# Kernel tuning notes

Measured on AMD Instinct MI355X. Metric: run time of the kernel, lower is better.

Reference implementation:

```python
import jax, jax.numpy as jnp
import numpy as np

# Fixed query graph: 3 terms, 3 predicates, edges (head_term, tail_term, pred):
# (0,1,0), (1,2,1), (0,2,2) -> every term has degree 2 -> seq_len 3 incl. self.
T, P, B, D, H, NL, FF = 3, 3, 16384, 256, 8, 2, 1024
DH = D // H
SCALE = DH ** -0.5


def setup_inputs() -> dict:
    key = jax.random.key(0)
    ks = jax.random.split(key, 8)
    s = 0.02
    f = jnp.float32
    return {
        "term_embs": jax.random.normal(ks[0], (T, B, D), f),
        "pred_embs": jax.random.normal(ks[1], (P, B, D), f),
        "Wq": jax.random.normal(ks[2], (NL, D, D), f) * s,
        "Wk": jax.random.normal(ks[3], (NL, D, D), f) * s,
        "Wv": jax.random.normal(ks[4], (NL, D, D), f) * s,
        "Wo": jax.random.normal(ks[5], (NL, D, D), f) * s,
        "bq": jnp.zeros((NL, D), f),
        "bk": jnp.zeros((NL, D), f),
        "bv": jnp.zeros((NL, D), f),
        "bo": jnp.zeros((NL, D), f),
        "ln1_g": jnp.ones((NL, D), f),
        "ln1_b": jnp.zeros((NL, D), f),
        "ln2_g": jnp.ones((NL, D), f),
        "ln2_b": jnp.zeros((NL, D), f),
        "W1": jax.random.normal(ks[6], (NL, D, FF), f) * s,
        "b1": jnp.zeros((NL, FF), f),
        "W2": jax.random.normal(ks[7], (NL, FF, D), f) * s,
        "b2": jnp.zeros((NL, D), f),
        "lnf_g": jnp.ones((D,), f),
        "lnf_b": jnp.zeros((D,), f),
    }


def _layer_norm(x, g, b):
    m = jnp.mean(x, axis=-1, keepdims=True)
    v = jnp.var(x, axis=-1, keepdims=True)
    return (x - m) * jax.lax.rsqrt(v + 1e-5) * g + b


def _forward(term_embs, pred_embs, Wq, Wk, Wv, Wo, bq, bk, bv, bo,
             ln1_g, ln1_b, ln2_g, ln2_b, W1, b1, W2, b2, lnf_g, lnf_b):
    # --- message passing (TransE-style NBP): tail_est = head + pred, head_est = tail - pred
    # edge heads: [0,1,0], edge tails: [1,2,2]
    tail_msgs = term_embs[jnp.array([0, 1, 0])] + pred_embs  # [P,B,D] -> sent to tail terms
    head_msgs = term_embs[jnp.array([1, 2, 2])] - pred_embs  # [P,B,D] -> sent to head terms
    # collect per term (static gather) + self embedding appended last
    x0 = jnp.stack([head_msgs[0], head_msgs[2], term_embs[0]], axis=1)  # [B,3,D]
    x1 = jnp.stack([tail_msgs[0], head_msgs[1], term_embs[1]], axis=1)
    x2 = jnp.stack([tail_msgs[1], tail_msgs[2], term_embs[2]], axis=1)
    x = jnp.concatenate([x0, x1, x2], axis=0)  # [T*B, 3, D]
    # --- pre-norm Transformer encoder, NL layers (dropout off at eval)
    for l in range(NL):
        h = _layer_norm(x, ln1_g[l], ln1_b[l])
        q = (h @ Wq[l] + bq[l]).reshape(-1, 3, H, DH)
        k = (h @ Wk[l] + bk[l]).reshape(-1, 3, H, DH)
        v = (h @ Wv[l] + bv[l]).reshape(-1, 3, H, DH)
        a = jax.nn.softmax(jnp.einsum('nqhd,nkhd->nhqk', q, k) * SCALE, axis=-1)
        o = jnp.einsum('nhqk,nkhd->nqhd', a, v).reshape(-1, 3, D)
        x = x + o @ Wo[l] + bo[l]
        h = _layer_norm(x, ln2_g[l], ln2_b[l])
        x = x + jax.nn.relu(h @ W1[l] + b1[l]) @ W2[l] + b2[l]
    x = _layer_norm(x, lnf_g, lnf_b)
    # --- aggregate (agg_func='mean') over the small message sequence
    return jnp.mean(x, axis=1).reshape(T, B, D)


def reference(term_embs, pred_embs, Wq, Wk, Wv, Wo, bq, bk, bv, bo,
              ln1_g, ln1_b, ln2_g, ln2_b, W1, b1, W2, b2, lnf_g, lnf_b):
    return _forward(term_embs, pred_embs, Wq, Wk, Wv, Wo, bq, bk, bv, bo,
                    ln1_g, ln1_b, ln2_g, ln2_b, W1, b1, W2, b2, lnf_g, lnf_b)
```

## Files before the change

### kernel.cpp

```cpp
#include <hip/hip_runtime.h>
#include <hip/hip_bf16.h>
#include <stdint.h>

typedef __hip_bfloat16 bf16;
typedef unsigned short u16;
typedef unsigned int u32;
typedef __bf16 v8bf __attribute__((ext_vector_type(8)));
typedef float v4f __attribute__((ext_vector_type(4)));

#define NB 16384
#define MROWS 147456

__device__ __forceinline__ float b2f(u16 u) {
  union { u32 u; float f; } v; v.u = ((u32)u) << 16; return v.f;
}
__device__ __forceinline__ u16 f2b(float f) {
  union { float f; u32 u; } v; v.f = f;
  u32 u = v.u;
  return (u16)((u + 0x7fffu + ((u >> 16) & 1u)) >> 16);
}
__device__ __forceinline__ void async16(const u16* g, u16* lds) {
  __builtin_amdgcn_global_load_lds((const __attribute__((address_space(1))) void*)g,
                                   (__attribute__((address_space(3))) void*)lds,
                                   16, 0, 0);
}
__device__ __forceinline__ v4f mfma16(v8bf a, v8bf b, v4f c) {
  return __builtin_amdgcn_mfma_f32_16x16x32_bf16(a, b, c, 0, 0, 0);
}

__device__ __forceinline__ v8bf ldsA256(const u16* As, int row, int k) {
  int byte = (row << 9) + ((k << 1) ^ ((row & 7) << 4));
  return *(const v8bf*)((const char*)As + byte);
}
__device__ __forceinline__ v8bf ldsB64(const u16* Bs, int row, int kb) {
  int byte = (row << 7) + (kb ^ ((row & 7) << 4));
  return *(const v8bf*)((const char*)Bs + byte);
}

__device__ __forceinline__ void so4_init(int tid, int S, int* so) {
  #pragma unroll
  for (int i = 0; i < 4; i++) {
    int b = (tid + i * 512) * 16;
    int r = b >> 7, ib = b & 127;
    so[i] = r * S + ((ib ^ ((r & 7) << 4)) >> 1);
  }
}
__device__ __forceinline__ void stage4(const u16* g, const int* so, u16* Bs, int tid) {
  #pragma unroll
  for (int i = 0; i < 4; i++)
    async16(g + so[i], Bs + tid * 8 + i * 4096);
}

__global__ __launch_bounds__(256)
void prep_weights(const float* Wq, const float* Wk, const float* Wv, const float* Wo,
                  const float* W1, const float* W2,
                  const float* bq, const float* bk, const float* bv,
                  bf16* wt, float* bqkv)
{
  if (blockIdx.x == 6144) {
    for (int e = threadIdx.x; e < 1536; e += 256) {
      int l = e / 768;
      int rem = e - l * 768;
      int wsel = rem >> 8;
      int col = rem & 255;
      const float* s = (wsel == 0) ? bq : (wsel == 1) ? bk : bv;
      bqkv[e] = s[l * 256 + col];
    }
    return;
  }
  int gid = blockIdx.x * 256 + threadIdx.x;
  int layer = (gid >= 786432) ? 1 : 0;
  int r = gid - layer * 786432;
  const float* src; int K, N, e, outoff;
  if (r < 262144) {
    int which = r >> 16;
    e = r & 65535; K = 256; N = 256;
    const float* w = (which == 0) ? Wq : (which == 1) ? Wk : (which == 2) ? Wv : Wo;
    src = w + layer * 65536;
    outoff = layer * 786432 + which * 65536;
  } else if (r < 524288) {
    e = r - 262144; K = 256; N = 1024;
    src = W1 + layer * 262144;
    outoff = layer * 786432 + 262144;
  } else {
    e = r - 524288; K = 1024; N = 256;
    src = W2 + layer * 262144;
    outoff = layer * 786432 + 524288;
  }
  int n = e / K, kk = e - n * K;
  ((u16*)wt)[outoff + e] = f2b(src[kk * N + n]);
}

__global__ __launch_bounds__(256)
void build_x(const float* __restrict__ T, const float* __restrict__ P,
             float* __restrict__ X, int row0)
{
  const int lane = threadIdx.x & 63;
  const int lrow = blockIdx.x * 4 + (threadIdx.x >> 6);
  const int row = row0 + lrow;
  const int d0 = lane * 4;
  int n = row / 3;
  int t = row - n * 3;
  float4 v;
  if (t == 2) {
    v = *(const float4*)(T + (size_t)n * 256 + d0);
  } else {
    int tm = n >> 14, b = n & 16383;
    const int srcT[6] = {1, 2,  0, 2,  1, 0};
    const int srcP[6] = {0, 2,  0, 1,  1, 2};
    const float sg[6] = {-1.f, -1.f,  1.f, -1.f,  1.f, 1.f};
    int idx = tm * 2 + t;
    float4 tv = *(const float4*)(T + ((size_t)(srcT[idx] * NB + b)) * 256 + d0);
    float4 pv = *(const float4*)(P + ((size_t)(srcP[idx] * NB + b)) * 256 + d0);
    float s = sg[idx];
    v.x = tv.x + s * pv.x;
    v.y = tv.y + s * pv.y;
    v.z = tv.z + s * pv.z;
    v.w = tv.w + s * pv.w;
  }
  *(float4*)(X + (size_t)lrow * 256 + d0) = v;
}

__device__ __forceinline__ void ln_stage(const float* __restrict__ xp,
                                         const float* __restrict__ gp,
                                         const float* __restrict__ bp,
                                         u16* As, int m0, int w, int lane)
{
  const float4 gv = *(const float4*)(gp + lane * 4);
  const float4 bv = *(const float4*)(bp + lane * 4);
  for (int r = w; r < 64; r += 8) {
    float4 v = *(const float4*)(xp + (size_t)(m0 + r) * 256 + lane * 4);
    float s = v.x + v.y + v.z + v.w;
    float q = v.x * v.x + v.y * v.y + v.z * v.z + v.w * v.w;
    #pragma unroll
    for (int m = 32; m > 0; m >>= 1) {
      s += __shfl_xor(s, m, 64);
      q += __shfl_xor(q, m, 64);
    }
    float mean = s * (1.f / 256.f);
    float var = q * (1.f / 256.f) - mean * mean;
    float rr = rsqrtf(var + 1e-5f);
    ushort4 o;
    o.x = f2b((v.x - mean) * rr * gv.x + bv.x);
    o.y = f2b((v.y - mean) * rr * gv.y + bv.y);
    o.z = f2b((v.z - mean) * rr * gv.z + bv.z);
    o.w = f2b((v.w - mean) * rr * gv.w + bv.w);
    int byte = (r << 9) + ((lane << 3) ^ ((r & 7) << 4));
    *(ushort4*)((char*)As + byte) = o;
  }
}

#define LOAD_AREGS(a, Src, fl, fh)                                  \
  _Pragma("unroll")                                                 \
  for (int mi = 0; mi < 4; mi++)                                    \
    _Pragma("unroll")                                               \
    for (int ks = 0; ks < 8; ks++)                                  \
      a[mi][ks] = ldsA256(Src, mi * 16 + fl, ks * 32 + fh * 8);

__global__ __launch_bounds__(512, 2)
void qkv_fused(const float* __restrict__ xp, const float* __restrict__ gp,
               const float* __restrict__ bp, const bf16* __restrict__ wp,
               const float* __restrict__ biasp, bf16* __restrict__ qkv,
               long long qkvZ)
{
  __shared__ __align__(16) u16 As[64 * 256];
  __shared__ __align__(16) u16 Bs[2 * 16384];
  const int tid = threadIdx.x;
  const int w = tid >> 6, lane = tid & 63;
  const int m0 = blockIdx.x * 64;
  const int fl = lane & 15, fh = lane >> 4;
  const int wc = w * 32;
  int so[4];
  so4_init(tid, 256, so);
  const u16* wp16 = (const u16*)wp;
  stage4(wp16, so, Bs, tid);
  ln_stage(xp, gp, bp, As, m0, w, lane);
  __syncthreads();
  v8bf a[4][8];
  LOAD_AREGS(a, As, fl, fh);
  #pragma unroll
  for (int wsel = 0; wsel < 3; wsel++) {
    v4f acc[4][2];
    #pragma unroll
    for (int mi = 0; mi < 4; mi++)
      #pragma unroll
      for (int nj = 0; nj < 2; nj++) { v4f z = {0.f,0.f,0.f,0.f}; acc[mi][nj] = z; }
    #pragma unroll
    for (int kt = 0; kt < 4; kt++) {
      const int t = wsel * 4 + kt;
      if (t + 1 < 12) {
        const int t1 = t + 1, ws1 = t1 >> 2, kt1 = t1 & 3;
        stage4(wp16 + ws1 * 65536 + kt1 * 64, so, Bs + (t1 & 1) * 16384, tid);
      }
      const u16* Bt = Bs + (t & 1) * 16384;
      #pragma unroll
      for (int kl = 0; kl < 2; kl++) {
        const int ksub = kt * 2 + kl;
        v8bf b0 = ldsB64(Bt, wc + fl, kl * 64 + fh * 16);
        v8bf b1 = ldsB64(Bt, wc + 16 + fl, kl * 64 + fh * 16);
        #pragma unroll
        for (int mi = 0; mi < 4; mi++) {
          acc[mi][0] = mfma16(a[mi][ksub], b0, acc[mi][0]);
          acc[mi][1] = mfma16(a[mi][ksub], b1, acc[mi][1]);
        }
      }
      __syncthreads();
    }
    u16* out = (u16*)qkv + (size_t)wsel * qkvZ;
    #pragma unroll
    for (int nj = 0; nj < 2; nj++) {
      const int col = wc + nj * 16 + fl;
      const float bb = biasp[wsel * 256 + col];
      #pragma unroll
      for (int mi = 0; mi < 4; mi++)
        #pragma unroll
        for (int r2 = 0; r2 < 4; r2++) {
          int row = m0 + mi * 16 + fh * 4 + r2;
          out[(size_t)row * 256 + col] = f2b(acc[mi][nj][r2] + bb);
        }
    }
  }
}

__global__ __launch_bounds__(512, 2)
void oproj(const bf16* __restrict__ op, const bf16* __restrict__ wop,
           const float* __restrict__ bop, float* __restrict__ xp)
{
  __shared__ __align__(16) u16 As[64 * 256];
  __shared__ __align__(16) u16 Bs[2 * 16384];
  const int tid = threadIdx.x;
  const int w = tid >> 6, lane = tid & 63;
  const int m0 = blockIdx.x * 64;
  const int fl = lane & 15, fh = lane >> 4;
  const int wc = w * 32;
  const u16* og = (const u16*)op + (size_t)m0 * 256;
  #pragma unroll
  for (int i = 0; i < 4; i++) {
    int b = i * 8192 + tid * 16;
    int row = b >> 9, cb = b & 511;
    int srce = row * 256 + ((cb ^ ((row & 7) << 4)) >> 1);
    async16(og + srce, As + (b >> 1));
  }
  int so[4];
  so4_init(tid, 256, so);
  const u16* wo16 = (const u16*)wop;
  stage4(wo16, so, Bs, tid);
  __syncthreads();
  v8bf a[4][8];
  LOAD_AREGS(a, As, fl, fh);
  v4f acc[4][2];
  #pragma unroll
  for (int mi = 0; mi < 4; mi++)
    #pragma unroll
    for (int nj = 0; nj < 2; nj++) { v4f z = {0.f,0.f,0.f,0.f}; acc[mi][nj] = z; }
  #pragma unroll
  for (int kt = 0; kt < 4; kt++) {
    if (kt + 1 < 4)
      stage4(wo16 + (kt + 1) * 64, so, Bs + ((kt + 1) & 1) * 16384, tid);
    const u16* Bt = Bs + (kt & 1) * 16384;
    #pragma unroll
    for (int kl = 0; kl < 2; kl++) {
      const int ksub = kt * 2 + kl;
      v8bf b0 = ldsB64(Bt, wc + fl, kl * 64 + fh * 16);
      v8bf b1 = ldsB64(Bt, wc + 16 + fl, kl * 64 + fh * 16);
      #pragma unroll
      for (int mi = 0; mi < 4; mi++) {
        acc[mi][0] = mfma16(a[mi][ksub], b0, acc[mi][0]);
        acc[mi][1] = mfma16(a[mi][ksub], b1, acc[mi][1]);
      }
    }
    __syncthreads();
  }
  #pragma unroll
  for (int nj = 0; nj < 2; nj++) {
    const int col = wc + nj * 16 + fl;
    const float bb = bop[col];
    #pragma unroll
    for (int mi = 0; mi < 4; mi++)
      #pragma unroll
      for (int r2 = 0; r2 < 4; r2++) {
        size_t idx = (size_t)(m0 + mi * 16 + fh * 4 + r2) * 256 + col;
        xp[idx] += acc[mi][nj][r2] + bb;
      }
  }
}

__global__ __launch_bounds__(512, 2)
void ffn_fused(float* __restrict__ xp, const float* __restrict__ gp,
               const float* __restrict__ bp, const bf16* __restrict__ w1p,
               const bf16* __restrict__ w2p, const float* __restrict__ b1p,
               const float* __restrict__ b2p)
{
  __shared__ __align__(16) u16 As[64 * 256];
  __shared__ __align__(16) u16 Fs[64 * 256];
  __shared__ __align__(16) u16 Bs[2 * 16384];
  const int tid = threadIdx.x;
  const int w = tid >> 6, lane = tid & 63;
  const int m0 = blockIdx.x * 64;
  const int fl = lane & 15, fh = lane >> 4;
  const int wc = w * 32;
  int so1[4], so2[4];
  so4_init(tid, 256, so1);
  so4_init(tid, 1024, so2);
  const u16* w1 = (const u16*)w1p;
  const u16* w2 = (const u16*)w2p;
  stage4(w1, so1, Bs, tid);
  ln_stage(xp, gp, bp, As, m0, w, lane);
  __syncthreads();
  v8bf a[4][8];
  LOAD_AREGS(a, As, fl, fh);
  v4f acc[4][2];
  #pragma unroll
  for (int mi = 0; mi < 4; mi++)
    #pragma unroll
    for (int nj = 0; nj < 2; nj++) { v4f z = {0.f,0.f,0.f,0.f}; acc[mi][nj] = z; }
  #pragma unroll
  for (int nc = 0; nc < 4; nc++) {
    v4f fa[4][2];
    #pragma unroll
    for (int mi = 0; mi < 4; mi++)
      #pragma unroll
      for (int nj = 0; nj < 2; nj++) { v4f z = {0.f,0.f,0.f,0.f}; fa[mi][nj] = z; }
    #pragma unroll
    for (int sub = 0; sub < 8; sub++) {
      const int t = nc * 8 + sub;
      if (t + 1 < 32) {
        const int t1 = t + 1, nc1 = t1 >> 3, sub1 = t1 & 7;
        u16* dst = Bs + (t1 & 1) * 16384;
        if (sub1 < 4) stage4(w1 + nc1 * 65536 + sub1 * 64, so1, dst, tid);
        else          stage4(w2 + nc1 * 256 + (sub1 - 4) * 64, so2, dst, tid);
      }
      const u16* Bt = Bs + (t & 1) * 16384;
      if (sub < 4) {
        #pragma unroll
        for (int kl = 0; kl < 2; kl++) {
          const int ksub = sub * 2 + kl;
          v8bf b0 = ldsB64(Bt, wc + fl, kl * 64 + fh * 16);
          v8bf b1 = ldsB64(Bt, wc + 16 + fl, kl * 64 + fh * 16);
          #pragma unroll
          for (int mi = 0; mi < 4; mi++) {
            fa[mi][0] = mfma16(a[mi][ksub], b0, fa[mi][0]);
            fa[mi][1] = mfma16(a[mi][ksub], b1, fa[mi][1]);
          }
        }
        if (sub == 3) {
          #pragma unroll
          for (int nj = 0; nj < 2; nj++) {
            const int colc = wc + nj * 16 + fl;
            const float bb = b1p[nc * 256 + colc];
            #pragma unroll
            for (int mi = 0; mi < 4; mi++)
              #pragma unroll
              for (int r2 = 0; r2 < 4; r2++) {
                int row = mi * 16 + fh * 4 + r2;
                float vv = fmaxf(fa[mi][nj][r2] + bb, 0.f);
                int byte = (row << 9) + (((colc << 1)) ^ ((row & 7) << 4));
                *(u16*)((char*)Fs + byte) = f2b(vv);
              }
          }
        }
      } else {
        const int ks = sub - 4;
        #pragma unroll
        for (int kl = 0; kl < 2; kl++) {
          v8bf b0 = ldsB64(Bt, wc + fl, kl * 64 + fh * 16);
          v8bf b1 = ldsB64(Bt, wc + 16 + fl, kl * 64 + fh * 16);
          #pragma unroll
          for (int mi = 0; mi < 4; mi++) {
            v8bf af = ldsA256(Fs, mi * 16 + fl, (ks * 2 + kl) * 32 + fh * 8);
            acc[mi][0] = mfma16(af, b0, acc[mi][0]);
            acc[mi][1] = mfma16(af, b1, acc[mi][1]);
          }
        }
      }
      __syncthreads();
    }
  }
  #pragma unroll
  for (int nj = 0; nj < 2; nj++) {
    const int col = wc + nj * 16 + fl;
    const float bb = b2p[col];
    #pragma unroll
    for (int mi = 0; mi < 4; mi++)
      #pragma unroll
      for (int r2 = 0; r2 < 4; r2++) {
        size_t idx = (size_t)(m0 + mi * 16 + fh * 4 + r2) * 256 + col;
        xp[idx] += acc[mi][nj][r2] + bb;
      }
  }
}

__global__ __launch_bounds__(256)
void attn(const bf16* __restrict__ qp, const bf16* __restrict__ kp,
          const bf16* __restrict__ vp, bf16* __restrict__ op)
{
  __shared__ __align__(16) u16 qs[6144], ks[6144], vs[6144];
  __shared__ float probs[8][8][9];
  const int tid = threadIdx.x;
  const size_t gbase = (size_t)blockIdx.x * 6144;
  const uint4* qg = (const uint4*)((const u16*)qp + gbase);
  const uint4* kg = (const uint4*)((const u16*)kp + gbase);
  const uint4* vg = (const uint4*)((const u16*)vp + gbase);
  for (int c = tid; c < 768; c += 256) {
    ((uint4*)qs)[c] = qg[c];
    ((uint4*)ks)[c] = kg[c];
    ((uint4*)vs)[c] = vg[c];
  }
  __syncthreads();
  if (tid < 64) {
    int s = tid >> 3, h = tid & 7;
    int base = s * 768 + h * 32;
    float sc[3][3];
    #pragma unroll
    for (int i = 0; i < 3; i++)
      #pragma unroll
      for (int j = 0; j < 3; j++) {
        float sum = 0.f;
        #pragma unroll
        for (int d = 0; d < 32; d++)
          sum += b2f(qs[base + i * 256 + d]) * b2f(ks[base + j * 256 + d]);
        sc[i][j] = sum * 0.17677669529663687f;
      }
    #pragma unroll
    for (int i = 0; i < 3; i++) {
      float m = fmaxf(sc[i][0], fmaxf(sc[i][1], sc[i][2]));
      float e0 = __expf(sc[i][0] - m);
      float e1 = __expf(sc[i][1] - m);
      float e2 = __expf(sc[i][2] - m);
      float inv = 1.f / (e0 + e1 + e2);
      probs[s][h][i * 3 + 0] = e0 * inv;
      probs[s][h][i * 3 + 1] = e1 * inv;
      probs[s][h][i * 3 + 2] = e2 * inv;
    }
  }
  __syncthreads();
  u16* og = (u16*)op + gbase;
  for (int c = tid; c < 6144; c += 256) {
    int lrow = c >> 8, hd = c & 255;
    int s = lrow / 3, i = lrow - s * 3;
    int h = hd >> 5;
    float p0 = probs[s][h][i * 3 + 0];
    float p1 = probs[s][h][i * 3 + 1];
    float p2 = probs[s][h][i * 3 + 2];
    float o = p0 * b2f(vs[s * 768 + hd])
            + p1 * b2f(vs[s * 768 + 256 + hd])
            + p2 * b2f(vs[s * 768 + 512 + hd]);
    og[c] = f2b(o);
  }
}

__global__ __launch_bounds__(256)
void ln_final_mean(const float* __restrict__ xp, const float* __restrict__ gp,
                   const float* __restrict__ bp, float* __restrict__ outp)
{
  const int lane = threadIdx.x & 63;
  const int n = blockIdx.x * 4 + (threadIdx.x >> 6);
  float4 gv = *(const float4*)(gp + lane * 4);
  float4 bv4 = *(const float4*)(bp + lane * 4);
  float a0 = 0.f, a1 = 0.f, a2 = 0.f, a3 = 0.f;
  for (int t = 0; t < 3; t++) {
    float4 rv = *(const float4*)(xp + ((size_t)n * 3 + t) * 256 + lane * 4);
    float v0 = rv.x, v1 = rv.y, v2 = rv.z, v3 = rv.w;
    float s = v0 + v1 + v2 + v3;
    float q = v0 * v0 + v1 * v1 + v2 * v2 + v3 * v3;
    #pragma unroll
    for (int m = 32; m > 0; m >>= 1) {
      s += __shfl_xor(s, m, 64);
      q += __shfl_xor(q, m, 64);
    }
    float mean = s * (1.f / 256.f);
    float var = q * (1.f / 256.f) - mean * mean;
    float r = rsqrtf(var + 1e-5f);
    a0 += (v0 - mean) * r * gv.x + bv4.x;
    a1 += (v1 - mean) * r * gv.y + bv4.y;
    a2 += (v2 - mean) * r * gv.z + bv4.z;
    a3 += (v3 - mean) * r * gv.w + bv4.w;
  }
  const float third = 1.f / 3.f;
  float4 outv;
  outv.x = a0 * third;
  outv.y = a1 * third;
  outv.z = a2 * third;
  outv.w = a3 * third;
  *(float4*)(outp + (size_t)n * 256 + lane * 4) = outv;
}

extern "C" void kernel_launch(void* const* d_in, const int* in_sizes, int n_in,
                              void* d_out, int out_size, void* d_ws, size_t ws_size,
                              hipStream_t stream)
{
  const float* term = (const float*)d_in[0];
  const float* pred = (const float*)d_in[1];
  const float* Wq  = (const float*)d_in[2];
  const float* Wk  = (const float*)d_in[3];
  const float* Wv  = (const float*)d_in[4];
  const float* Wo  = (const float*)d_in[5];
  const float* bq  = (const float*)d_in[6];
  const float* bk  = (const float*)d_in[7];
  const float* bvv = (const float*)d_in[8];
  const float* bo  = (const float*)d_in[9];
  const float* ln1g = (const float*)d_in[10];
  const float* ln1b = (const float*)d_in[11];
  const float* ln2g = (const float*)d_in[12];
  const float* ln2b = (const float*)d_in[13];
  const float* W1  = (const float*)d_in[14];
  const float* b1  = (const float*)d_in[15];
  const float* W2  = (const float*)d_in[16];
  const float* b2  = (const float*)d_in[17];
  const float* lnfg = (const float*)d_in[18];
  const float* lnfb = (const float*)d_in[19];

  int nch = 128;
  for (int c = 2; c <= 128; c *= 2) {
    size_t Mc_ = (size_t)MROWS / c;
    size_t need = 4ull * 1024 * 1024 + Mc_ * 3072ull;
    if (need <= ws_size) { nch = c; break; }
  }
  const size_t Mc = (size_t)MROWS / nch;

  char* ws = (char*)d_ws;
  bf16* wt   = (bf16*)ws;
  float* bqkv = (float*)(ws + 3145728);
  float* x = (float*)(ws + 4194304);
  bf16* q = (bf16*)(x + Mc * 256);
  bf16* v_ = q + 2 * Mc * 256;
  bf16* o = q + 3 * Mc * 256;

  prep_weights<<<6145, 256, 0, stream>>>(Wq, Wk, Wv, Wo, W1, W2, bq, bk, bvv, wt, bqkv);

  const long long qkvZ = (long long)(Mc * 256);
  for (int ch = 0; ch < nch; ch++) {
    const int row0 = (int)(ch * Mc);
    build_x<<<(int)(Mc / 4), 256, 0, stream>>>(term, pred, x, row0);
    for (int l = 0; l < 2; l++) {
      const bf16* wl = wt + (size_t)l * 786432;
      qkv_fused<<<(int)(Mc / 64), 512, 0, stream>>>(
          x, ln1g + l * 256, ln1b + l * 256, wl, bqkv + l * 768, q, qkvZ);
      attn<<<(int)(Mc / 24), 256, 0, stream>>>(q, q + Mc * 256, v_, o);
      oproj<<<(int)(Mc / 64), 512, 0, stream>>>(o, wl + 196608, bo + l * 256, x);
      ffn_fused<<<(int)(Mc / 64), 512, 0, stream>>>(
          x, ln2g + l * 256, ln2b + l * 256, wl + 262144, wl + 524288,
          b1 + l * 1024, b2 + l * 256);
    }
    ln_final_mean<<<(int)(Mc / 12), 256, 0, stream>>>(
        x, lnfg, lnfb, (float*)d_out + (size_t)(row0 / 3) * 256);
  }
}
```

Before: 1.533 ms.

## Restructure GEMM kernels to 4-wave blocks with wider per-wave tiles and explicit waitcnt pipelining

The QKV, output-projection and FFN GEMM kernels now run 256-thread blocks instead of 512, and each wave computes a 64-column tile (4x4 MFMA accumulators) instead of 32. The A operand is streamed from LDS per k-step rather than held entirely in registers, and the weight tiles are staged in smaller 32-wide k slices. Double buffering now uses explicit vmcnt waits and raw s_barrier calls with sched barriers in place of __syncthreads. The FFN hidden chunk drops from 256 to 128, which shrinks the LDS footprint. The aim is better B-tile reuse and lower register and LDS pressure, at the cost of fewer waves per block to hide latency and more barrier steps.

```diff
diff --git a/kernel.cpp b/kernel.cpp
--- a/kernel.cpp
+++ b/kernel.cpp
@@ -11,6 +11,12 @@
 #define NB 16384
 #define MROWS 147456
 
+#define VMWAIT4 do { asm volatile("s_waitcnt vmcnt(4)" ::: "memory"); } while (0)
+#define VMWAIT0 do { asm volatile("s_waitcnt vmcnt(0)" ::: "memory"); } while (0)
+#define LGKM0   do { asm volatile("s_waitcnt lgkmcnt(0)" ::: "memory"); } while (0)
+#define SCHEDB  __builtin_amdgcn_sched_barrier(0)
+#define SBAR    __builtin_amdgcn_s_barrier()
+
 __device__ __forceinline__ float b2f(u16 u) {
   union { u32 u; float f; } v; v.u = ((u32)u) << 16; return v.f;
 }
@@ -32,23 +38,39 @@
   int byte = (row << 9) + ((k << 1) ^ ((row & 7) << 4));
   return *(const v8bf*)((const char*)As + byte);
 }
+__device__ __forceinline__ v8bf ldsF128(const u16* Fs, int row, int k) {
+  int byte = (row << 8) + ((k << 1) ^ ((row & 7) << 4));
+  return *(const v8bf*)((const char*)Fs + byte);
+}
 __device__ __forceinline__ v8bf ldsB64(const u16* Bs, int row, int kb) {
   int byte = (row << 7) + (kb ^ ((row & 7) << 4));
   return *(const v8bf*)((const char*)Bs + byte);
 }
-
-__device__ __forceinline__ void so4_init(int tid, int S, int* so) {
+__device__ __forceinline__ v8bf ldsB32(const u16* Bs, int row, int kb) {
+  int byte = (row << 6) + (kb ^ (((row >> 1) & 3) << 4));
+  return *(const v8bf*)((const char*)Bs + byte);
+}
+
+__device__ __forceinline__ void soB32_init(int tid, int S, int* so) {
   #pragma unroll
   for (int i = 0; i < 4; i++) {
-    int b = (tid + i * 512) * 16;
+    int b = tid * 16 + i * 4096;
+    int r = b >> 6, ib = b & 63;
+    so[i] = r * S + ((ib ^ (((r >> 1) & 3) << 4)) >> 1);
+  }
+}
+__device__ __forceinline__ void soB64_init(int tid, int S, int* so) {
+  #pragma unroll
+  for (int i = 0; i < 4; i++) {
+    int b = tid * 16 + i * 4096;
     int r = b >> 7, ib = b & 127;
     so[i] = r * S + ((ib ^ ((r & 7) << 4)) >> 1);
   }
 }
-__device__ __forceinline__ void stage4(const u16* g, const int* so, u16* Bs, int tid) {
+__device__ __forceinline__ void stageB(const u16* g, const int* so, u16* dst, int tid) {
   #pragma unroll
   for (int i = 0; i < 4; i++)
-    async16(g + so[i], Bs + tid * 8 + i * 4096);
+    async16(g + so[i], dst + tid * 8 + i * 2048);
 }
 
 __global__ __launch_bounds__(256)
@@ -128,7 +150,7 @@
 {
   const float4 gv = *(const float4*)(gp + lane * 4);
   const float4 bv = *(const float4*)(bp + lane * 4);
-  for (int r = w; r < 64; r += 8) {
+  for (int r = w; r < 64; r += 4) {
     float4 v = *(const float4*)(xp + (size_t)(m0 + r) * 256 + lane * 4);
     float s = v.x + v.y + v.z + v.w;
     float q = v.x * v.x + v.y * v.y + v.z * v.z + v.w * v.w;
@@ -150,65 +172,63 @@
   }
 }
 
-#define LOAD_AREGS(a, Src, fl, fh)                                  \
-  _Pragma("unroll")                                                 \
-  for (int mi = 0; mi < 4; mi++)                                    \
-    _Pragma("unroll")                                               \
-    for (int ks = 0; ks < 8; ks++)                                  \
-      a[mi][ks] = ldsA256(Src, mi * 16 + fl, ks * 32 + fh * 8);
-
-__global__ __launch_bounds__(512, 2)
+__global__ __launch_bounds__(256, 2)
 void qkv_fused(const float* __restrict__ xp, const float* __restrict__ gp,
                const float* __restrict__ bp, const bf16* __restrict__ wp,
                const float* __restrict__ biasp, bf16* __restrict__ qkv,
                long long qkvZ)
 {
   __shared__ __align__(16) u16 As[64 * 256];
-  __shared__ __align__(16) u16 Bs[2 * 16384];
+  __shared__ __align__(16) u16 Bs[2 * 8192];
   const int tid = threadIdx.x;
   const int w = tid >> 6, lane = tid & 63;
   const int m0 = blockIdx.x * 64;
   const int fl = lane & 15, fh = lane >> 4;
-  const int wc = w * 32;
+  const int wc = w * 64;
   int so[4];
-  so4_init(tid, 256, so);
+  soB32_init(tid, 256, so);
   const u16* wp16 = (const u16*)wp;
-  stage4(wp16, so, Bs, tid);
+  stageB(wp16, so, Bs, tid);
   ln_stage(xp, gp, bp, As, m0, w, lane);
   __syncthreads();
-  v8bf a[4][8];
-  LOAD_AREGS(a, As, fl, fh);
-  #pragma unroll
+  #pragma unroll 1
   for (int wsel = 0; wsel < 3; wsel++) {
-    v4f acc[4][2];
+    v4f acc[4][4];
     #pragma unroll
     for (int mi = 0; mi < 4; mi++)
       #pragma unroll
-      for (int nj = 0; nj < 2; nj++) { v4f z = {0.f,0.f,0.f,0.f}; acc[mi][nj] = z; }
-    #pragma unroll
-    for (int kt = 0; kt < 4; kt++) {
-      const int t = wsel * 4 + kt;
-      if (t + 1 < 12) {
-        const int t1 = t + 1, ws1 = t1 >> 2, kt1 = t1 & 3;
-        stage4(wp16 + ws1 * 65536 + kt1 * 64, so, Bs + (t1 & 1) * 16384, tid);
-      }
-      const u16* Bt = Bs + (t & 1) * 16384;
-      #pragma unroll
-      for (int kl = 0; kl < 2; kl++) {
-        const int ksub = kt * 2 + kl;
-        v8bf b0 = ldsB64(Bt, wc + fl, kl * 64 + fh * 16);
-        v8bf b1 = ldsB64(Bt, wc + 16 + fl, kl * 64 + fh * 16);
-        #pragma unroll
-        for (int mi = 0; mi < 4; mi++) {
-          acc[mi][0] = mfma16(a[mi][ksub], b0, acc[mi][0]);
-          acc[mi][1] = mfma16(a[mi][ksub], b1, acc[mi][1]);
-        }
-      }
-      __syncthreads();
+      for (int nj = 0; nj < 4; nj++) { v4f z = {0.f,0.f,0.f,0.f}; acc[mi][nj] = z; }
+    #pragma unroll
+    for (int ks = 0; ks < 8; ks++) {
+      u16* nbuf = Bs + (((ks + 1) & 1) * 8192);
+      if (ks < 7) {
+        stageB(wp16 + wsel * 65536 + (ks + 1) * 32, so, nbuf, tid);
+        VMWAIT4;
+      } else if (wsel < 2) {
+        stageB(wp16 + (wsel + 1) * 65536, so, nbuf, tid);
+        VMWAIT4;
+      } else {
+        VMWAIT0;
+      }
+      SCHEDB; SBAR; SCHEDB;
+      const u16* Bt = Bs + (ks & 1) * 8192;
+      v8bf a0 = ldsA256(As, 0 * 16 + fl, ks * 32 + fh * 8);
+      v8bf a1 = ldsA256(As, 1 * 16 + fl, ks * 32 + fh * 8);
+      v8bf a2 = ldsA256(As, 2 * 16 + fl, ks * 32 + fh * 8);
+      v8bf a3 = ldsA256(As, 3 * 16 + fl, ks * 32 + fh * 8);
+      #pragma unroll
+      for (int nj = 0; nj < 4; nj++) {
+        v8bf b = ldsB32(Bt, wc + nj * 16 + fl, fh * 16);
+        acc[0][nj] = mfma16(a0, b, acc[0][nj]);
+        acc[1][nj] = mfma16(a1, b, acc[1][nj]);
+        acc[2][nj] = mfma16(a2, b, acc[2][nj]);
+        acc[3][nj] = mfma16(a3, b, acc[3][nj]);
+      }
+      SCHEDB; SBAR;
     }
     u16* out = (u16*)qkv + (size_t)wsel * qkvZ;
     #pragma unroll
-    for (int nj = 0; nj < 2; nj++) {
+    for (int nj = 0; nj < 4; nj++) {
       const int col = wc + nj * 16 + fl;
       const float bb = biasp[wsel * 256 + col];
       #pragma unroll
@@ -222,57 +242,61 @@
   }
 }
 
-__global__ __launch_bounds__(512, 2)
+__global__ __launch_bounds__(256, 2)
 void oproj(const bf16* __restrict__ op, const bf16* __restrict__ wop,
            const float* __restrict__ bop, float* __restrict__ xp)
 {
   __shared__ __align__(16) u16 As[64 * 256];
-  __shared__ __align__(16) u16 Bs[2 * 16384];
+  __shared__ __align__(16) u16 Bs[2 * 8192];
   const int tid = threadIdx.x;
   const int w = tid >> 6, lane = tid & 63;
   const int m0 = blockIdx.x * 64;
   const int fl = lane & 15, fh = lane >> 4;
-  const int wc = w * 32;
+  const int wc = w * 64;
   const u16* og = (const u16*)op + (size_t)m0 * 256;
   #pragma unroll
-  for (int i = 0; i < 4; i++) {
-    int b = i * 8192 + tid * 16;
+  for (int i = 0; i < 8; i++) {
+    int b = tid * 16 + i * 4096;
     int row = b >> 9, cb = b & 511;
     int srce = row * 256 + ((cb ^ ((row & 7) << 4)) >> 1);
     async16(og + srce, As + (b >> 1));
   }
   int so[4];
-  so4_init(tid, 256, so);
+  soB32_init(tid, 256, so);
   const u16* wo16 = (const u16*)wop;
-  stage4(wo16, so, Bs, tid);
+  stageB(wo16, so, Bs, tid);
   __syncthreads();
-  v8bf a[4][8];
-  LOAD_AREGS(a, As, fl, fh);
-  v4f acc[4][2];
+  v4f acc[4][4];
   #pragma unroll
   for (int mi = 0; mi < 4; mi++)
     #pragma unroll
-    for (int nj = 0; nj < 2; nj++) { v4f z = {0.f,0.f,0.f,0.f}; acc[mi][nj] = z; }
-  #pragma unroll
-  for (int kt = 0; kt < 4; kt++) {
-    if (kt + 1 < 4)
-      stage4(wo16 + (kt + 1) * 64, so, Bs + ((kt + 1) & 1) * 16384, tid);
-    const u16* Bt = Bs + (kt & 1) * 16384;
-    #pragma unroll
-    for (int kl = 0; kl < 2; kl++) {
-      const int ksub = kt * 2 + kl;
-      v8bf b0 = ldsB64(Bt, wc + fl, kl * 64 + fh * 16);
-      v8bf b1 = ldsB64(Bt, wc + 16 + fl, kl * 64 + fh * 16);
-      #pragma unroll
-      for (int mi = 0; mi < 4; mi++) {
-        acc[mi][0] = mfma16(a[mi][ksub], b0, acc[mi][0]);
-        acc[mi][1] = mfma16(a[mi][ksub], b1, acc[mi][1]);
-      }
-    }
-    __syncthreads();
-  }
-  #pragma unroll
-  for (int nj = 0; nj < 2; nj++) {
+    for (int nj = 0; nj < 4; nj++) { v4f z = {0.f,0.f,0.f,0.f}; acc[mi][nj] = z; }
+  #pragma unroll
+  for (int ks = 0; ks < 8; ks++) {
+    if (ks < 7) {
+      stageB(wo16 + (ks + 1) * 32, so, Bs + (((ks + 1) & 1) * 8192), tid);
+      VMWAIT4;
+    } else {
+      VMWAIT0;
+    }
+    SCHEDB; SBAR; SCHEDB;
+    const u16* Bt = Bs + (ks & 1) * 8192;
+    v8bf a0 = ldsA256(As, 0 * 16 + fl, ks * 32 + fh * 8);
+    v8bf a1 = ldsA256(As, 1 * 16 + fl, ks * 32 + fh * 8);
+    v8bf a2 = ldsA256(As, 2 * 16 + fl, ks * 32 + fh * 8);
+    v8bf a3 = ldsA256(As, 3 * 16 + fl, ks * 32 + fh * 8);
+    #pragma unroll
+    for (int nj = 0; nj < 4; nj++) {
+      v8bf b = ldsB32(Bt, wc + nj * 16 + fl, fh * 16);
+      acc[0][nj] = mfma16(a0, b, acc[0][nj]);
+      acc[1][nj] = mfma16(a1, b, acc[1][nj]);
+      acc[2][nj] = mfma16(a2, b, acc[2][nj]);
+      acc[3][nj] = mfma16(a3, b, acc[3][nj]);
+    }
+    SCHEDB; SBAR;
+  }
+  #pragma unroll
+  for (int nj = 0; nj < 4; nj++) {
     const int col = wc + nj * 16 + fl;
     const float bb = bop[col];
     #pragma unroll
@@ -285,37 +309,36 @@
   }
 }
 
-__global__ __launch_bounds__(512, 2)
+__global__ __launch_bounds__(256, 2)
 void ffn_fused(float* __restrict__ xp, const float* __restrict__ gp,
                const float* __restrict__ bp, const bf16* __restrict__ w1p,
                const bf16* __restrict__ w2p, const float* __restrict__ b1p,
                const float* __restrict__ b2p)
 {
   __shared__ __align__(16) u16 As[64 * 256];
-  __shared__ __align__(16) u16 Fs[64 * 256];
-  __shared__ __align__(16) u16 Bs[2 * 16384];
+  __shared__ __align__(16) u16 Fs[64 * 128];
+  __shared__ __align__(16) u16 Bs[2 * 8192];
   const int tid = threadIdx.x;
   const int w = tid >> 6, lane = tid & 63;
   const int m0 = blockIdx.x * 64;
   const int fl = lane & 15, fh = lane >> 4;
-  const int wc = w * 32;
+  const int wc1 = w * 32;
+  const int wc2 = w * 64;
   int so1[4], so2[4];
-  so4_init(tid, 256, so1);
-  so4_init(tid, 1024, so2);
+  soB64_init(tid, 256, so1);
+  soB32_init(tid, 1024, so2);
   const u16* w1 = (const u16*)w1p;
   const u16* w2 = (const u16*)w2p;
-  stage4(w1, so1, Bs, tid);
+  stageB(w1, so1, Bs, tid);
   ln_stage(xp, gp, bp, As, m0, w, lane);
   __syncthreads();
-  v8bf a[4][8];
-  LOAD_AREGS(a, As, fl, fh);
-  v4f acc[4][2];
+  v4f acc[4][4];
   #pragma unroll
   for (int mi = 0; mi < 4; mi++)
     #pragma unroll
-    for (int nj = 0; nj < 2; nj++) { v4f z = {0.f,0.f,0.f,0.f}; acc[mi][nj] = z; }
-  #pragma unroll
-  for (int nc = 0; nc < 4; nc++) {
+    for (int nj = 0; nj < 4; nj++) { v4f z = {0.f,0.f,0.f,0.f}; acc[mi][nj] = z; }
+  #pragma unroll 1
+  for (int nc = 0; nc < 8; nc++) {
     v4f fa[4][2];
     #pragma unroll
     for (int mi = 0; mi < 4; mi++)
@@ -323,62 +346,78 @@
       for (int nj = 0; nj < 2; nj++) { v4f z = {0.f,0.f,0.f,0.f}; fa[mi][nj] = z; }
     #pragma unroll
     for (int sub = 0; sub < 8; sub++) {
-      const int t = nc * 8 + sub;
-      if (t + 1 < 32) {
-        const int t1 = t + 1, nc1 = t1 >> 3, sub1 = t1 & 7;
-        u16* dst = Bs + (t1 & 1) * 16384;
-        if (sub1 < 4) stage4(w1 + nc1 * 65536 + sub1 * 64, so1, dst, tid);
-        else          stage4(w2 + nc1 * 256 + (sub1 - 4) * 64, so2, dst, tid);
-      }
-      const u16* Bt = Bs + (t & 1) * 16384;
+      u16* nbuf = Bs + (((sub + 1) & 1) * 8192);
+      if (sub < 3) {
+        stageB(w1 + nc * 32768 + (sub + 1) * 64, so1, nbuf, tid);
+        VMWAIT4;
+      } else if (sub < 7) {
+        stageB(w2 + nc * 128 + (sub - 3) * 32, so2, nbuf, tid);
+        VMWAIT4;
+      } else if (nc < 7) {
+        stageB(w1 + (nc + 1) * 32768, so1, nbuf, tid);
+        VMWAIT4;
+      } else {
+        VMWAIT0;
+      }
+      SCHEDB; SBAR; SCHEDB;
+      const u16* Bt = Bs + (sub & 1) * 8192;
       if (sub < 4) {
         #pragma unroll
         for (int kl = 0; kl < 2; kl++) {
-          const int ksub = sub * 2 + kl;
-          v8bf b0 = ldsB64(Bt, wc + fl, kl * 64 + fh * 16);
-          v8bf b1 = ldsB64(Bt, wc + 16 + fl, kl * 64 + fh * 16);
-          #pragma unroll
-          for (int mi = 0; mi < 4; mi++) {
-            fa[mi][0] = mfma16(a[mi][ksub], b0, fa[mi][0]);
-            fa[mi][1] = mfma16(a[mi][ksub], b1, fa[mi][1]);
-          }
+          const int kA = sub * 64 + kl * 32 + fh * 8;
+          v8bf a0 = ldsA256(As, 0 * 16 + fl, kA);
+          v8bf a1 = ldsA256(As, 1 * 16 + fl, kA);
+          v8bf a2 = ldsA256(As, 2 * 16 + fl, kA);
+          v8bf a3 = ldsA256(As, 3 * 16 + fl, kA);
+          v8bf b0 = ldsB64(Bt, wc1 + fl, kl * 64 + fh * 16);
+          v8bf b1 = ldsB64(Bt, wc1 + 16 + fl, kl * 64 + fh * 16);
+          fa[0][0] = mfma16(a0, b0, fa[0][0]);
+          fa[1][0] = mfma16(a1, b0, fa[1][0]);
+          fa[2][0] = mfma16(a2, b0, fa[2][0]);
+          fa[3][0] = mfma16(a3, b0, fa[3][0]);
+          fa[0][1] = mfma16(a0, b1, fa[0][1]);
+          fa[1][1] = mfma16(a1, b1, fa[1][1]);
+          fa[2][1] = mfma16(a2, b1, fa[2][1]);
+          fa[3][1] = mfma16(a3, b1, fa[3][1]);
         }
         if (sub == 3) {
           #pragma unroll
           for (int nj = 0; nj < 2; nj++) {
-            const int colc = wc + nj * 16 + fl;
-            const float bb = b1p[nc * 256 + colc];
+            const int colc = wc1 + nj * 16 + fl;
+            const float bb = b1p[nc * 128 + colc];
             #pragma unroll
             for (int mi = 0; mi < 4; mi++)
               #pragma unroll
               for (int r2 = 0; r2 < 4; r2++) {
                 int row = mi * 16 + fh * 4 + r2;
                 float vv = fmaxf(fa[mi][nj][r2] + bb, 0.f);
-                int byte = (row << 9) + (((colc << 1)) ^ ((row & 7) << 4));
+                int byte = (row << 8) + (((colc << 1)) ^ ((row & 7) << 4));
                 *(u16*)((char*)Fs + byte) = f2b(vv);
               }
           }
+          LGKM0; SCHEDB;
         }
       } else {
         const int ks = sub - 4;
+        v8bf f0 = ldsF128(Fs, 0 * 16 + fl, ks * 32 + fh * 8);
+        v8bf f1 = ldsF128(Fs, 1 * 16 + fl, ks * 32 + fh * 8);
+        v8bf f2 = ldsF128(Fs, 2 * 16 + fl, ks * 32 + fh * 8);
+        v8bf f3 = ldsF128(Fs, 3 * 16 + fl, ks * 32 + fh * 8);
         #pragma unroll
-        for (int kl = 0; kl < 2; kl++) {
-          v8bf b0 = ldsB64(Bt, wc + fl, kl * 64 + fh * 16);
-          v8bf b1 = ldsB64(Bt, wc + 16 + fl, kl * 64 + fh * 16);
-          #pragma unroll
-          for (int mi = 0; mi < 4; mi++) {
-            v8bf af = ldsA256(Fs, mi * 16 + fl, (ks * 2 + kl) * 32 + fh * 8);
-            acc[mi][0] = mfma16(af, b0, acc[mi][0]);
-            acc[mi][1] = mfma16(af, b1, acc[mi][1]);
-          }
+        for (int nj = 0; nj < 4; nj++) {
+          v8bf b = ldsB32(Bt, wc2 + nj * 16 + fl, fh * 16);
+          acc[0][nj] = mfma16(f0, b, acc[0][nj]);
+          acc[1][nj] = mfma16(f1, b, acc[1][nj]);
+          acc[2][nj] = mfma16(f2, b, acc[2][nj]);
+          acc[3][nj] = mfma16(f3, b, acc[3][nj]);
         }
       }
-      __syncthreads();
-    }
-  }
-  #pragma unroll
-  for (int nj = 0; nj < 2; nj++) {
-    const int col = wc + nj * 16 + fl;
+      SCHEDB; SBAR;
+    }
+  }
+  #pragma unroll
+  for (int nj = 0; nj < 4; nj++) {
+    const int col = wc2 + nj * 16 + fl;
     const float bb = b2p[col];
     #pragma unroll
     for (int mi = 0; mi < 4; mi++)
@@ -534,11 +573,11 @@
     build_x<<<(int)(Mc / 4), 256, 0, stream>>>(term, pred, x, row0);
     for (int l = 0; l < 2; l++) {
       const bf16* wl = wt + (size_t)l * 786432;
-      qkv_fused<<<(int)(Mc / 64), 512, 0, stream>>>(
+      qkv_fused<<<(int)(Mc / 64), 256, 0, stream>>>(
           x, ln1g + l * 256, ln1b + l * 256, wl, bqkv + l * 768, q, qkvZ);
       attn<<<(int)(Mc / 24), 256, 0, stream>>>(q, q + Mc * 256, v_, o);
-      oproj<<<(int)(Mc / 64), 512, 0, stream>>>(o, wl + 196608, bo + l * 256, x);
-      ffn_fused<<<(int)(Mc / 64), 512, 0, stream>>>(
+      oproj<<<(int)(Mc / 64), 256, 0, stream>>>(o, wl + 196608, bo + l * 256, x);
+      ffn_fused<<<(int)(Mc / 64), 256, 0, stream>>>(
           x, ln2g + l * 256, ln2b + l * 256, wl + 262144, wl + 524288,
           b1 + l * 1024, b2 + l * 256);
     }
```

Result: no change. 1.564 ms (+2.0%).
